# Optimization experiments

Hardware: AMD Instinct MI355X
Metric: run time of the kernel (lower is better)

## Reference

```python
import jax, jax.numpy as jnp
import numpy as np

B, S, HID = 1, 2048, 2048
H, KVH, D = 16, 8, 128
QR, KR, VR = 6, 2, 2
SOFTCAP = 50.0
SCALING = D ** -0.5
NEG = -1e9


def _rope(Bfac, cos, sin):
    # Bfac: [b, s, r, d]; cos/sin: [s, d//2]; rotates adjacent pairs (complex view)
    x = Bfac.reshape(*Bfac.shape[:-1], D // 2, 2)
    xe, xo = x[..., 0], x[..., 1]
    c = cos[None, :, None, :]
    s = sin[None, :, None, :]
    oe = xe * c - xo * s
    oo = xe * s + xo * c
    return jnp.stack([oe, oo], axis=-1).reshape(Bfac.shape)


def setup_inputs() -> dict:
    key = jax.random.key(0)
    ks = jax.random.split(key, 12)
    hidden_states = jax.random.normal(ks[0], (B, S, HID), jnp.float32)
    # rotary tables (standard RoPE frequencies)
    inv_freq = 1.0 / (10000.0 ** (jnp.arange(0, D, 2, dtype=jnp.float32) / D))
    t = jnp.arange(S, dtype=jnp.float32)
    ang = t[:, None] * inv_freq[None, :]            # [S, D//2]
    cos, sin = jnp.cos(ang), jnp.sin(ang)
    # causal additive mask [1,1,S,S]
    causal = jnp.tril(jnp.ones((S, S), bool))
    mask = jnp.where(causal, 0.0, NEG).astype(jnp.float32)[None, None]
    kv_write_indices = jnp.arange(S, dtype=jnp.int32)
    sc = lambda k, shp: jax.random.normal(k, shp, jnp.float32) * (shp[0] ** -0.5)
    return {
        "hidden_states": hidden_states, "cos": cos, "sin": sin, "mask": mask,
        "kv_write_indices": kv_write_indices,
        "WAq": sc(ks[1], (HID, H * QR)), "WAk": sc(ks[2], (HID, KVH * KR)),
        "WAv": sc(ks[3], (HID, KVH * VR)), "WBq": sc(ks[4], (HID, QR * D)),
        "WBk": sc(ks[5], (HID, KR * D)), "WBv": sc(ks[6], (HID, VR * D)),
        "Wo": sc(ks[7], (H * D, HID)),
    }


def reference(hidden_states, cos, sin, mask, kv_write_indices,
              WAq, WAk, WAv, WBq, WBk, WBv, Wo):
    b, s, _ = hidden_states.shape
    # factor projections (never materialize full Q/K/V)
    A_q = (hidden_states @ WAq).reshape(b, s, H, QR)
    A_k = (hidden_states @ WAk).reshape(b, s, KVH, KR)
    A_v = (hidden_states @ WAv).reshape(b, s, KVH, VR)
    B_q = (hidden_states @ WBq).reshape(b, s, QR, D)
    B_k = (hidden_states @ WBk).reshape(b, s, KR, D)
    B_v = (hidden_states @ WBv).reshape(b, s, VR, D)
    # RoPE on B factors
    B_q = _rope(B_q, cos, sin)
    B_k = _rope(B_k, cos, sin)
    # prefill: kv_write_indices = arange(S) => cache slices equal current factors
    # GQA: broadcast KV heads up to H
    hpk = H // KVH
    A_k = jnp.repeat(A_k, hpk, axis=2)   # [b,k,H,KR]
    A_v = jnp.repeat(A_v, hpk, axis=2)   # [b,k,H,VR]
    # factor-expanded attention scores
    B_dots = jnp.einsum('bqrd,bksd->bqkrs', B_q, B_k) * SCALING
    attn = jnp.einsum('bqhr,bkhs,bqkrs->bhqk', A_q, A_k, B_dots)
    # logit softcapping
    attn = SOFTCAP * jnp.tanh(attn / SOFTCAP)
    attn = attn + mask
    probs = jax.nn.softmax(attn.astype(jnp.float32), axis=-1).astype(hidden_states.dtype)
    # factor-expanded output
    out = jnp.einsum('bhqk,bkhu,bkud->bhqd', probs, A_v, B_v)
    out = out.transpose(0, 2, 1, 3).reshape(b, s, H * D)
    return out @ Wo
```

## Files before the change

### kernel.cpp

```cpp
#include <hip/hip_runtime.h>


constexpr int SEQ   = 2048;
constexpr int HIDN  = 2048;
constexpr int NHEAD = 16;
constexpr int NKVH  = 8;
constexpr int DH    = 128;
constexpr int NCOLS = 1408;

typedef __bf16 bf16x8 __attribute__((ext_vector_type(8)));
typedef float  f32x4  __attribute__((ext_vector_type(4)));

#define MFMA(a, b, c) __builtin_amdgcn_mfma_f32_16x16x32_bf16((a), (b), (c), 0, 0, 0)

__device__ __forceinline__ void gload_lds16(const void* g, void* l) {
  __builtin_amdgcn_global_load_lds(
      (const __attribute__((address_space(1))) void*)g,
      (__attribute__((address_space(3))) void*)l, 16, 0, 0);
}


__global__ __launch_bounds__(256) void k_prep(
    const float* __restrict__ hidden,
    const float* __restrict__ WAq, const float* __restrict__ WAk,
    const float* __restrict__ WAv, const float* __restrict__ WBq,
    const float* __restrict__ WBk, const float* __restrict__ WBv,
    __bf16* __restrict__ hid_bf, __bf16* __restrict__ WT) {
  const int bid = blockIdx.x;
  if (bid < 2048) {
    const int i = (bid * 256 + threadIdx.x) * 8;
    f32x4 a = *(const f32x4*)(hidden + i);
    f32x4 b = *(const f32x4*)(hidden + i + 4);
    bf16x8 v;
#pragma unroll
    for (int j = 0; j < 4; j++) { v[j] = (__bf16)a[j]; v[4 + j] = (__bf16)b[j]; }
    *(bf16x8*)(hid_bf + i) = v;
  } else {
    const int t = bid - 2048;
    const int bc = (t % 44) * 32, bk = (t / 44) * 32;
    __shared__ float tl[32][33];
    const int tx = threadIdx.x & 31, ty = threadIdx.x >> 5;
    const int c = bc + tx;
#pragma unroll
    for (int j = 0; j < 32; j += 8) {
      const int k = bk + ty + j;
      float v;
      if (c < 96)        v = WAq[k * 96 + c];
      else if (c < 112)  v = WAk[k * 16 + (c - 96)];
      else if (c < 128)  v = WAv[k * 16 + (c - 112)];
      else if (c < 896)  v = WBq[k * 768 + (c - 128)];
      else if (c < 1152) v = WBk[k * 256 + (c - 896)];
      else               v = WBv[k * 256 + (c - 1152)];
      tl[ty + j][tx] = v;
    }
    __syncthreads();
#pragma unroll
    for (int j = 0; j < 32; j += 8)
      WT[(size_t)(bc + ty + j) * HIDN + bk + tx] = (__bf16)tl[tx][ty + j];
  }
}


__global__ __launch_bounds__(256) void k_proj_wo(
    const __bf16* __restrict__ A, const __bf16* __restrict__ BT,
    float* __restrict__ C, const float* __restrict__ Wo,
    __bf16* __restrict__ WoT) {
  __shared__ char smem[49152];
  const int bid = blockIdx.x;
  if (bid >= 352) {
    const int t = bid - 352;
    const int bn = (t % 64) * 32, bk = (t / 64) * 32;
    float (*tl)[33] = (float(*)[33])smem;
    const int tx = threadIdx.x & 31, ty = threadIdx.x >> 5;
#pragma unroll
    for (int j = 0; j < 32; j += 8)
      tl[ty + j][tx] = Wo[(size_t)(bk + ty + j) * HIDN + bn + tx];
    __syncthreads();
#pragma unroll
    for (int j = 0; j < 32; j += 8)
      WoT[(size_t)(bn + ty + j) * HIDN + bk + tx] = (__bf16)tl[tx][ty + j];
    return;
  }
  const int K = HIDN, N = NCOLS;
  __bf16* As = (__bf16*)smem;
  __bf16* Bs = (__bf16*)(smem + 32768);
  const int tid = threadIdx.x;
  const int w = tid >> 6, lane = tid & 63;
  const int lhi = lane >> 4, llo = lane & 15;
  const int wr = w >> 1, wc = w & 1;
  const int sid = (bid & 7) * 44 + (bid >> 3);
  const int brow = (sid / 22) * 128, bcol = (sid % 22) * 64;
  const int rA = lane >> 2, kA = (lane & 3) * 8;
  const int nt = K >> 5;

  f32x4 acc[4][2];
#pragma unroll
  for (int m = 0; m < 4; m++)
#pragma unroll
    for (int n = 0; n < 2; n++) acc[m][n] = (f32x4){0.f, 0.f, 0.f, 0.f};

  auto stage = [&](int t) {
    const int buf = t & 3;
    const int k0 = t * 32;
#pragma unroll
    for (int i = 0; i < 2; i++) {
      int seg = w * 2 + i;
      int row = seg * 16 + rA;
      gload_lds16(A + (size_t)(brow + row) * K + k0 + kA,
                  As + buf * 4096 + seg * 512);
    }
    gload_lds16(BT + (size_t)(bcol + w * 16 + rA) * K + k0 + kA,
                Bs + buf * 2048 + w * 512);
  };

  stage(0); stage(1); stage(2);
  asm volatile("s_waitcnt vmcnt(6)" ::: "memory");
  __builtin_amdgcn_s_barrier();

  for (int t = 0; t < nt; t++) {
    if (t + 3 < nt) stage(t + 3);
    const int buf = t & 3;
    bf16x8 af[4], bfr[2];
#pragma unroll
    for (int m = 0; m < 4; m++)
      af[m] = *(const bf16x8*)&As[buf * 4096 + (wr * 64 + m * 16 + llo) * 32 + lhi * 8];
#pragma unroll
    for (int n = 0; n < 2; n++)
      bfr[n] = *(const bf16x8*)&Bs[buf * 2048 + (wc * 32 + n * 16 + llo) * 32 + lhi * 8];
#pragma unroll
    for (int m = 0; m < 4; m++)
#pragma unroll
      for (int n = 0; n < 2; n++) acc[m][n] = MFMA(af[m], bfr[n], acc[m][n]);
    const int rem = nt - 2 - t;
    if (rem >= 2)      asm volatile("s_waitcnt vmcnt(6)" ::: "memory");
    else if (rem == 1) asm volatile("s_waitcnt vmcnt(3)" ::: "memory");
    else               asm volatile("s_waitcnt vmcnt(0)" ::: "memory");
    __builtin_amdgcn_s_barrier();
  }

#pragma unroll
  for (int m = 0; m < 4; m++)
#pragma unroll
    for (int n = 0; n < 2; n++) {
      int r0 = brow + wr * 64 + m * 16 + lhi * 4;
      int c0 = bcol + wc * 32 + n * 16 + llo;
#pragma unroll
      for (int r = 0; r < 4; r++) C[(size_t)(r0 + r) * N + c0] = acc[m][n][r];
    }
}


__global__ __launch_bounds__(512) void k_gemm_out(const __bf16* __restrict__ A,
                                                  const __bf16* __restrict__ BT,
                                                  float* __restrict__ C) {
  __shared__ __bf16 As[4][4096];
  __shared__ __bf16 Bs[4][4096];
  const int K = HIDN, N = HIDN;
  const int tid = threadIdx.x;
  const int w = tid >> 6, lane = tid & 63;
  const int lhi = lane >> 4, llo = lane & 15;
  const int wr = w >> 2, wc = w & 3;

  const int id = blockIdx.y * 16 + blockIdx.x;
  const int g = id & 7, kk = id >> 3;
  const int rg = g >> 2, cg = g & 3;
  const int brow = (rg * 8 + (kk & 7)) * 128;
  const int bcol = (cg * 4 + (kk >> 3)) * 128;

  const int rA = tid >> 2, kA = (tid & 3) * 8;
  const int nt = K >> 5;

  f32x4 acc[4][2];
#pragma unroll
  for (int m = 0; m < 4; m++)
#pragma unroll
    for (int n = 0; n < 2; n++) acc[m][n] = (f32x4){0.f, 0.f, 0.f, 0.f};

  auto stage = [&](int t) {
    const int buf = t & 3;
    const int k0 = t * 32;
    gload_lds16(A  + (size_t)(brow + rA) * K + k0 + kA, &As[buf][w * 512]);
    gload_lds16(BT + (size_t)(bcol + rA) * K + k0 + kA, &Bs[buf][w * 512]);
  };

  stage(0); stage(1); stage(2);
  asm volatile("s_waitcnt vmcnt(4)" ::: "memory");
  __builtin_amdgcn_s_barrier();

  for (int t = 0; t < nt; t++) {
    if (t + 3 < nt) stage(t + 3);
    const int buf = t & 3;
    bf16x8 af[4], bfr[2];
#pragma unroll
    for (int m = 0; m < 4; m++)
      af[m] = *(const bf16x8*)&As[buf][(wr * 64 + m * 16 + llo) * 32 + lhi * 8];
#pragma unroll
    for (int n = 0; n < 2; n++)
      bfr[n] = *(const bf16x8*)&Bs[buf][(wc * 32 + n * 16 + llo) * 32 + lhi * 8];
#pragma unroll
    for (int m = 0; m < 4; m++)
#pragma unroll
      for (int n = 0; n < 2; n++) acc[m][n] = MFMA(af[m], bfr[n], acc[m][n]);
    const int rem = nt - 2 - t;
    if (rem >= 2)      asm volatile("s_waitcnt vmcnt(4)" ::: "memory");
    else if (rem == 1) asm volatile("s_waitcnt vmcnt(2)" ::: "memory");
    else               asm volatile("s_waitcnt vmcnt(0)" ::: "memory");
    __builtin_amdgcn_s_barrier();
  }

#pragma unroll
  for (int m = 0; m < 4; m++)
#pragma unroll
    for (int n = 0; n < 2; n++) {
      int r0 = brow + wr * 64 + m * 16 + lhi * 4;
      int c0 = bcol + wc * 32 + n * 16 + llo;
#pragma unroll
      for (int r = 0; r < 4; r++) C[(size_t)(r0 + r) * N + c0] = acc[m][n][r];
    }
}


__global__ __launch_bounds__(128) void k_build_qkv(const float* __restrict__ P,
                                                   const float* __restrict__ cosT,
                                                   const float* __restrict__ sinT,
                                                   __bf16* __restrict__ Qo,
                                                   __bf16* __restrict__ Ko,
                                                   __bf16* __restrict__ Vto) {
  const int q = blockIdx.x, d = threadIdx.x;
  __shared__ float Ash[128];
  const float* row = P + (size_t)q * NCOLS;
  Ash[d] = row[d];
  __syncthreads();
  const int m2 = (d >> 1) * 2;
  const bool odd = d & 1;
  const float c = cosT[q * 64 + (d >> 1)];
  const float s = sinT[q * 64 + (d >> 1)];

  float qacc[16];
#pragma unroll
  for (int h = 0; h < 16; h++) qacc[h] = 0.f;
#pragma unroll
  for (int r = 0; r < 6; r++) {
    float xe = row[128 + r * 128 + m2];
    float xo = row[128 + r * 128 + m2 + 1];
    float br = odd ? (xe * s + xo * c) : (xe * c - xo * s);
#pragma unroll
    for (int h = 0; h < 16; h++) qacc[h] += Ash[h * 6 + r] * br;
  }
#pragma unroll
  for (int h = 0; h < 16; h++)
    Qo[((size_t)h * SEQ + q) * DH + d] = (__bf16)(qacc[h] * 0.08838834764831845f);

  float kacc[8];
#pragma unroll
  for (int g = 0; g < 8; g++) kacc[g] = 0.f;
#pragma unroll
  for (int ss = 0; ss < 2; ss++) {
    float xe = row[896 + ss * 128 + m2];
    float xo = row[896 + ss * 128 + m2 + 1];
    float bs = odd ? (xe * s + xo * c) : (xe * c - xo * s);
#pragma unroll
    for (int g = 0; g < 8; g++) kacc[g] += Ash[96 + g * 2 + ss] * bs;
  }
#pragma unroll
  for (int g = 0; g < 8; g++)
    Ko[((size_t)g * SEQ + q) * DH + d] = (__bf16)kacc[g];

  float vacc[8];
#pragma unroll
  for (int g = 0; g < 8; g++) vacc[g] = 0.f;
#pragma unroll
  for (int u = 0; u < 2; u++) {
    float vu = row[1152 + u * 128 + d];
#pragma unroll
    for (int g = 0; g < 8; g++) vacc[g] += Ash[112 + g * 2 + u] * vu;
  }
#pragma unroll
  for (int g = 0; g < 8; g++)
    Vto[((size_t)g * DH + d) * SEQ + q] = (__bf16)vacc[g];
}


__global__ __launch_bounds__(256) void k_attn(const __bf16* __restrict__ Q,
                                              const __bf16* __restrict__ Kc,
                                              const __bf16* __restrict__ Vt,
                                              float* __restrict__ AOf0,
                                              float* __restrict__ AOf1,
                                              float* __restrict__ Ls) {
  const int raw = blockIdx.x;
  const int g = raw & 7;
  const int j = raw >> 3;
  const int bqi = 31 - (j >> 2);
  const int hh = (j >> 1) & 1;
  const int p = j & 1;
  const int h = g * 2 + hh;
  const int w = threadIdx.x >> 6, lane = threadIdx.x & 63;
  const int lhi = lane >> 4, llo = lane & 15;
  const int q0 = bqi * 64 + w * 16;
  const int t0 = p * (bqi + 1), t1 = t0 + bqi + 1;

  __shared__ __bf16 KVs[2][8192];

  const __bf16* Qh = Q  + (size_t)h * SEQ * DH;
  const __bf16* Kg = Kc + (size_t)g * SEQ * DH;
  const __bf16* Vg = Vt + (size_t)g * DH * SEQ;
  float* AOc = p ? AOf1 : AOf0;

  bf16x8 aq[4];
#pragma unroll
  for (int c = 0; c < 4; c++)
    aq[c] = *(const bf16x8*)&Qh[(size_t)(q0 + llo) * DH + c * 32 + lhi * 8];

  f32x4 oacc[8];
  float lsum = 0.f;
#pragma unroll
  for (int n = 0; n < 8; n++) oacc[n] = (f32x4){0.f, 0.f, 0.f, 0.f};

  const int swv = (llo >> 1) & 3;
  const int vb0 = ((((lhi >> 1) ^ swv) << 4) | ((lhi & 1) << 3)) + llo * 64;
  const int vb1 = (((((lhi >> 1) + 2) ^ swv) << 4) | ((lhi & 1) << 3)) + llo * 64;

  auto stage = [&](int kb, int buf) {
    __bf16* L = KVs[buf];
    if (w < 2) {
#pragma unroll
      for (int u = 0; u < 4; u++) {
        int c = w * 256 + u * 64 + lane;
        int row = c >> 4, jj = c & 15;
        gload_lds16(Kg + (size_t)(kb + row) * DH + ((jj ^ (row & 7)) * 8),
                    L + (w * 256 + u * 64) * 8);
      }
    } else {
#pragma unroll
      for (int u = 0; u < 4; u++) {
        int c = (w - 2) * 256 + u * 64 + lane;
        int d = c >> 2, jj = c & 3;
        gload_lds16(Vg + (size_t)d * SEQ + kb + ((jj ^ ((d >> 1) & 3)) * 8),
                    L + 4096 + ((w - 2) * 256 + u * 64) * 8);
      }
    }
  };

  stage(t0 * 32, t0 & 1);
  for (int t = t0; t < t1; t++) {
    const int kb = t * 32;
    const int buf = t & 1;
    if (t + 1 < t1) {
      stage(kb + 32, buf ^ 1);
      asm volatile("s_waitcnt vmcnt(4)" ::: "memory");
    } else {
      asm volatile("s_waitcnt vmcnt(0)" ::: "memory");
    }
    __builtin_amdgcn_s_barrier();
    if (kb <= q0 + 15) {
      const char* Kl = (const char*)KVs[buf];
      const char* Vl = (const char*)(KVs[buf] + 4096);
      f32x4 s0 = {0.f, 0.f, 0.f, 0.f}, s1 = {0.f, 0.f, 0.f, 0.f};
#pragma unroll
      for (int c = 0; c < 4; c++) {
        const int row0 = llo, row1 = 16 + llo;
        bf16x8 k0 = *(const bf16x8*)(Kl + row0 * 256 +
                                     ((c * 64 + lhi * 16) ^ ((row0 & 7) << 4)));
        bf16x8 k1 = *(const bf16x8*)(Kl + row1 * 256 +
                                     ((c * 64 + lhi * 16) ^ ((row1 & 7) << 4)));
        s0 = MFMA(k0, aq[c], s0);
        s1 = MFMA(k1, aq[c], s1);
      }
      float e[8];
#pragma unroll
      for (int r = 0; r < 4; r++) {
        float a0 = exp2f(s0[r] * 0.057707802f);
        float a1 = exp2f(s1[r] * 0.057707802f);
        e[r]     = exp2f(72.134752f - 144.269504f * __builtin_amdgcn_rcpf(a0 + 1.f));
        e[4 + r] = exp2f(72.134752f - 144.269504f * __builtin_amdgcn_rcpf(a1 + 1.f));
      }
      if (kb + 31 > q0) {
        const int qrow = q0 + llo;
#pragma unroll
        for (int r = 0; r < 4; r++) {
          if (kb + lhi * 4 + r > qrow)      e[r] = 0.f;
          if (kb + 16 + lhi * 4 + r > qrow) e[4 + r] = 0.f;
        }
      }
#pragma unroll
      for (int r = 0; r < 4; r++) lsum += e[r] + e[4 + r];
      union { bf16x8 v8; unsigned u[4]; } pu;
      asm("v_cvt_pk_bf16_f32 %0, %1, %2" : "=v"(pu.u[0]) : "v"(e[0]), "v"(e[1]));
      asm("v_cvt_pk_bf16_f32 %0, %1, %2" : "=v"(pu.u[1]) : "v"(e[2]), "v"(e[3]));
      asm("v_cvt_pk_bf16_f32 %0, %1, %2" : "=v"(pu.u[2]) : "v"(e[4]), "v"(e[5]));
      asm("v_cvt_pk_bf16_f32 %0, %1, %2" : "=v"(pu.u[3]) : "v"(e[6]), "v"(e[7]));
#pragma unroll
      for (int n = 0; n < 8; n++) {
        union { bf16x8 v8; struct { uint2 lo, hi; } d; } vu;
        vu.d.lo = *(const uint2*)(Vl + vb0 + n * 1024);
        vu.d.hi = *(const uint2*)(Vl + vb1 + n * 1024);
        oacc[n] = MFMA(pu.v8, vu.v8, oacc[n]);
      }
    }
    asm volatile("" ::: "memory");
    __builtin_amdgcn_s_barrier();
  }

  float tsum = lsum;
  tsum += __shfl_xor(tsum, 16);
  tsum += __shfl_xor(tsum, 32);
  if (lhi == 0) Ls[((size_t)p * NHEAD + h) * SEQ + q0 + llo] = tsum;
#pragma unroll
  for (int r = 0; r < 4; r++) {
    const int qrow = q0 + lhi * 4 + r;
#pragma unroll
    for (int n = 0; n < 8; n++)
      AOc[(size_t)qrow * HIDN + h * DH + n * 16 + llo] = oacc[n][r];
  }
}


__global__ __launch_bounds__(256) void k_norm(const float* __restrict__ A0,
                                              const float* __restrict__ A1,
                                              const float* __restrict__ Ls,
                                              __bf16* __restrict__ AO) {
  const int i = (blockIdx.x * 256 + threadIdx.x) * 4;
  const int q = i >> 11, h = (i & 2047) >> 7;
  const float inv = 1.f / (Ls[h * SEQ + q] + Ls[(NHEAD + h) * SEQ + q]);
  f32x4 a = *(const f32x4*)(A0 + i);
  f32x4 b = *(const f32x4*)(A1 + i);
#pragma unroll
  for (int j = 0; j < 4; j++) AO[i + j] = (__bf16)((a[j] + b[j]) * inv);
}


extern "C" void kernel_launch(void* const* d_in, const int* in_sizes, int n_in,
                              void* d_out, int out_size, void* d_ws, size_t ws_size,
                              hipStream_t stream) {
  const float* hidden = (const float*)d_in[0];
  const float* cosT   = (const float*)d_in[1];
  const float* sinT   = (const float*)d_in[2];
  const float* WAq = (const float*)d_in[5];
  const float* WAk = (const float*)d_in[6];
  const float* WAv = (const float*)d_in[7];
  const float* WBq = (const float*)d_in[8];
  const float* WBk = (const float*)d_in[9];
  const float* WBv = (const float*)d_in[10];
  const float* Wo  = (const float*)d_in[11];
  float* out = (float*)d_out;

  char* ws = (char*)d_ws;
  __bf16* hid_bf = (__bf16*)(ws);
  __bf16* WallT  = (__bf16*)(ws + 8388608);
  float*  Pproj  = (float*)(ws + 14155776);
  __bf16* WoT    = (__bf16*)(ws + 25690112);
  __bf16* Qb     = (__bf16*)(ws + 34078720);
  __bf16* Kb     = (__bf16*)(ws + 42467328);
  __bf16* Vt     = (__bf16*)(ws + 46661632);
  float*  AOf0   = (float*)(ws);
  float*  AOf1   = (float*)(ws + 50855936);
  float*  Ls     = (float*)(ws + 67633152);
  __bf16* AO     = (__bf16*)(ws + 34078720);

  k_prep<<<2048 + 44 * 64, 256, 0, stream>>>(
      hidden, WAq, WAk, WAv, WBq, WBk, WBv, hid_bf, WallT);
  k_proj_wo<<<352 + 4096, 256, 0, stream>>>(hid_bf, WallT, Pproj, Wo, WoT);
  k_build_qkv<<<SEQ, 128, 0, stream>>>(Pproj, cosT, sinT, Qb, Kb, Vt);
  k_attn<<<1024, 256, 0, stream>>>(Qb, Kb, Vt, AOf0, AOf1, Ls);
  k_norm<<<(SEQ * HIDN / 4) / 256, 256, 0, stream>>>(AOf0, AOf1, Ls, AO);
  k_gemm_out<<<dim3(16, 16), 512, 0, stream>>>(AO, WoT, out);
}
```

Measured before the change: 153.7 us.

## Split-K the projection GEMM and permute V layout for single 128-bit LDS reads

The projection GEMM is split into two K halves, which doubles the block count from 352 to 704 to improve occupancy across the CUs. The two partial results are written to separate buffers and summed when the QKV build kernel reads them. V^T is also stored with a permuted sequence order inside each 32-key block, so attention can fetch its V MFMA operand as one bf16x8 LDS load instead of two 64-bit loads. This adds extra fp32 partial traffic and a second read in build_qkv, and it depends on the permutation exactly matching the MFMA k-ordering of P.

Result: faster. 149.5 us (-2.7%).

```diff
diff --git a/kernel.cpp b/kernel.cpp
--- a/kernel.cpp
+++ b/kernel.cpp
@@ -63,12 +63,12 @@
 
 __global__ __launch_bounds__(256) void k_proj_wo(
     const __bf16* __restrict__ A, const __bf16* __restrict__ BT,
-    float* __restrict__ C, const float* __restrict__ Wo,
-    __bf16* __restrict__ WoT) {
+    float* __restrict__ C0, float* __restrict__ C1,
+    const float* __restrict__ Wo, __bf16* __restrict__ WoT) {
   __shared__ char smem[49152];
   const int bid = blockIdx.x;
-  if (bid >= 352) {
-    const int t = bid - 352;
+  if (bid >= 704) {
+    const int t = bid - 704;
     const int bn = (t % 64) * 32, bk = (t / 64) * 32;
     float (*tl)[33] = (float(*)[33])smem;
     const int tx = threadIdx.x & 31, ty = threadIdx.x >> 5;
@@ -88,10 +88,14 @@
   const int w = tid >> 6, lane = tid & 63;
   const int lhi = lane >> 4, llo = lane & 15;
   const int wr = w >> 1, wc = w & 1;
-  const int sid = (bid & 7) * 44 + (bid >> 3);
+  const int z = (bid >= 352);
+  const int b = bid - z * 352;
+  float* C = z ? C1 : C0;
+  const int kbase = z * (K >> 1);
+  const int sid = (b & 7) * 44 + (b >> 3);
   const int brow = (sid / 22) * 128, bcol = (sid % 22) * 64;
   const int rA = lane >> 2, kA = (lane & 3) * 8;
-  const int nt = K >> 5;
+  const int nt = K >> 6;
 
   f32x4 acc[4][2];
 #pragma unroll
@@ -101,7 +105,7 @@
 
   auto stage = [&](int t) {
     const int buf = t & 3;
-    const int k0 = t * 32;
+    const int k0 = kbase + t * 32;
 #pragma unroll
     for (int i = 0; i < 2; i++) {
       int seg = w * 2 + i;
@@ -220,7 +224,8 @@
 }
 
 
-__global__ __launch_bounds__(128) void k_build_qkv(const float* __restrict__ P,
+__global__ __launch_bounds__(128) void k_build_qkv(const float* __restrict__ P0,
+                                                   const float* __restrict__ P1,
                                                    const float* __restrict__ cosT,
                                                    const float* __restrict__ sinT,
                                                    __bf16* __restrict__ Qo,
@@ -228,8 +233,10 @@
                                                    __bf16* __restrict__ Vto) {
   const int q = blockIdx.x, d = threadIdx.x;
   __shared__ float Ash[128];
-  const float* row = P + (size_t)q * NCOLS;
-  Ash[d] = row[d];
+  const float* r0 = P0 + (size_t)q * NCOLS;
+  const float* r1 = P1 + (size_t)q * NCOLS;
+  auto rd = [&](int i) { return r0[i] + r1[i]; };
+  Ash[d] = rd(d);
   __syncthreads();
   const int m2 = (d >> 1) * 2;
   const bool odd = d & 1;
@@ -241,8 +248,8 @@
   for (int h = 0; h < 16; h++) qacc[h] = 0.f;
 #pragma unroll
   for (int r = 0; r < 6; r++) {
-    float xe = row[128 + r * 128 + m2];
-    float xo = row[128 + r * 128 + m2 + 1];
+    float xe = rd(128 + r * 128 + m2);
+    float xo = rd(128 + r * 128 + m2 + 1);
     float br = odd ? (xe * s + xo * c) : (xe * c - xo * s);
 #pragma unroll
     for (int h = 0; h < 16; h++) qacc[h] += Ash[h * 6 + r] * br;
@@ -256,8 +263,8 @@
   for (int g = 0; g < 8; g++) kacc[g] = 0.f;
 #pragma unroll
   for (int ss = 0; ss < 2; ss++) {
-    float xe = row[896 + ss * 128 + m2];
-    float xo = row[896 + ss * 128 + m2 + 1];
+    float xe = rd(896 + ss * 128 + m2);
+    float xo = rd(896 + ss * 128 + m2 + 1);
     float bs = odd ? (xe * s + xo * c) : (xe * c - xo * s);
 #pragma unroll
     for (int g = 0; g < 8; g++) kacc[g] += Ash[96 + g * 2 + ss] * bs;
@@ -271,13 +278,14 @@
   for (int g = 0; g < 8; g++) vacc[g] = 0.f;
 #pragma unroll
   for (int u = 0; u < 2; u++) {
-    float vu = row[1152 + u * 128 + d];
+    float vu = rd(1152 + u * 128 + d);
 #pragma unroll
     for (int g = 0; g < 8; g++) vacc[g] += Ash[112 + g * 2 + u] * vu;
   }
+  const int qp = (q & ~31) | (((q & 15) >> 2) * 8 + (q & 3) + ((q & 16) >> 2));
 #pragma unroll
   for (int g = 0; g < 8; g++)
-    Vto[((size_t)g * DH + d) * SEQ + q] = (__bf16)vacc[g];
+    Vto[((size_t)g * DH + d) * SEQ + qp] = (__bf16)vacc[g];
 }
 
 
@@ -316,9 +324,7 @@
 #pragma unroll
   for (int n = 0; n < 8; n++) oacc[n] = (f32x4){0.f, 0.f, 0.f, 0.f};
 
-  const int swv = (llo >> 1) & 3;
-  const int vb0 = ((((lhi >> 1) ^ swv) << 4) | ((lhi & 1) << 3)) + llo * 64;
-  const int vb1 = (((((lhi >> 1) + 2) ^ swv) << 4) | ((lhi & 1) << 3)) + llo * 64;
+  const int vb = llo * 64 + ((lhi ^ ((llo >> 1) & 3)) << 4);
 
   auto stage = [&](int kb, int buf) {
     __bf16* L = KVs[buf];
@@ -391,10 +397,8 @@
       asm("v_cvt_pk_bf16_f32 %0, %1, %2" : "=v"(pu.u[3]) : "v"(e[6]), "v"(e[7]));
 #pragma unroll
       for (int n = 0; n < 8; n++) {
-        union { bf16x8 v8; struct { uint2 lo, hi; } d; } vu;
-        vu.d.lo = *(const uint2*)(Vl + vb0 + n * 1024);
-        vu.d.hi = *(const uint2*)(Vl + vb1 + n * 1024);
-        oacc[n] = MFMA(pu.v8, vu.v8, oacc[n]);
+        bf16x8 vf = *(const bf16x8*)(Vl + vb + n * 1024);
+        oacc[n] = MFMA(pu.v8, vf, oacc[n]);
       }
     }
     asm volatile("" ::: "memory");
@@ -447,11 +451,12 @@
   char* ws = (char*)d_ws;
   __bf16* hid_bf = (__bf16*)(ws);
   __bf16* WallT  = (__bf16*)(ws + 8388608);
-  float*  Pproj  = (float*)(ws + 14155776);
+  float*  Pp0    = (float*)(ws + 14155776);
   __bf16* WoT    = (__bf16*)(ws + 25690112);
   __bf16* Qb     = (__bf16*)(ws + 34078720);
   __bf16* Kb     = (__bf16*)(ws + 42467328);
   __bf16* Vt     = (__bf16*)(ws + 46661632);
+  float*  Pp1    = (float*)(ws + 50855936);
   float*  AOf0   = (float*)(ws);
   float*  AOf1   = (float*)(ws + 50855936);
   float*  Ls     = (float*)(ws + 67633152);
@@ -459,8 +464,8 @@
 
   k_prep<<<2048 + 44 * 64, 256, 0, stream>>>(
       hidden, WAq, WAk, WAv, WBq, WBk, WBv, hid_bf, WallT);
-  k_proj_wo<<<352 + 4096, 256, 0, stream>>>(hid_bf, WallT, Pproj, Wo, WoT);
-  k_build_qkv<<<SEQ, 128, 0, stream>>>(Pproj, cosT, sinT, Qb, Kb, Vt);
+  k_proj_wo<<<704 + 4096, 256, 0, stream>>>(hid_bf, WallT, Pp0, Pp1, Wo, WoT);
+  k_build_qkv<<<SEQ, 128, 0, stream>>>(Pp0, Pp1, cosT, sinT, Qb, Kb, Vt);
   k_attn<<<1024, 256, 0, stream>>>(Qb, Kb, Vt, AOf0, AOf1, Ls);
   k_norm<<<(SEQ * HIDN / 4) / 256, 256, 0, stream>>>(AOf0, AOf1, Ls, AO);
   k_gemm_out<<<dim3(16, 16), 512, 0, stream>>>(AO, WoT, out);
```
